# Kernel tuning notes

Measured on AMD Instinct MI355X. Metric: run time of the kernel, lower is better.

## Reference

```python
import jax, jax.numpy as jnp
import numpy as np

N = 50000      # nodes
E = 800000     # edges (before self-loops)
IN = 64        # in_dim
C = 64         # hidden_dim (per-head out channels)
H = 4          # heads
NEG_SLOPE = 0.2


def setup_inputs() -> dict:
    key = jax.random.key(0)
    ks = jax.random.split(key, 9)
    x = jax.random.normal(ks[0], (N, IN), jnp.float32)
    edge_index = jax.random.randint(ks[1], (2, E), 0, N)
    edge_attr = jax.random.uniform(ks[2], (E, 1), jnp.float32)
    s_in = 1.0 / np.sqrt(IN)
    s_c = 1.0 / np.sqrt(C)
    W = jax.random.normal(ks[3], (IN, H * C), jnp.float32) * s_in
    att_src = jax.random.normal(ks[4], (H, C), jnp.float32) * s_c
    att_dst = jax.random.normal(ks[5], (H, C), jnp.float32) * s_c
    lin_edge_w = jax.random.normal(ks[6], (1, H * C), jnp.float32)
    att_edge = jax.random.normal(ks[7], (H, C), jnp.float32) * s_c
    bias = jnp.zeros((C,), jnp.float32)
    return dict(x=x, edge_index=edge_index, edge_attr=edge_attr, W=W,
                att_src=att_src, att_dst=att_dst, lin_edge_w=lin_edge_w,
                att_edge=att_edge, bias=bias)


def reference(x, edge_index, edge_attr, W, att_src, att_dst, lin_edge_w, att_edge, bias):
    n = x.shape[0]
    # add self-loops (PyG default add_self_loops=True, fill_value='mean')
    loop = jnp.arange(n)
    src = jnp.concatenate([edge_index[0], loop])          # [E+N]
    dst = jnp.concatenate([edge_index[1], loop])          # [E+N]
    ea = jnp.concatenate([edge_attr,
                          jnp.full((n, 1), edge_attr.mean(), edge_attr.dtype)], axis=0)
    # node transform: [N, H, C]
    h = (x @ W).reshape(n, H, C)
    a_src = jnp.einsum('nhc,hc->nh', h, att_src)          # [N, H]
    a_dst = jnp.einsum('nhc,hc->nh', h, att_dst)          # [N, H]
    eh = (ea @ lin_edge_w).reshape(-1, H, C)              # [E+N, H, C]
    a_edge = jnp.einsum('ehc,hc->eh', eh, att_edge)       # [E+N, H]
    # per-edge attention logit
    alpha = a_src[src] + a_dst[dst] + a_edge              # [E+N, H]
    alpha = jax.nn.leaky_relu(alpha, NEG_SLOPE)
    # segment softmax over edges grouped by destination node
    amax = jax.ops.segment_max(alpha, dst, num_segments=n)
    alpha = jnp.exp(alpha - amax[dst])
    asum = jax.ops.segment_sum(alpha, dst, num_segments=n)
    alpha = alpha / (asum[dst] + 1e-16)                   # [E+N, H]
    # weighted message + scatter-add aggregation
    msg = h[src] * alpha[..., None]                       # [E+N, H, C]
    out = jax.ops.segment_sum(msg, dst, num_segments=n)   # [N, H, C]
    out = out.mean(axis=1) + bias                         # concat=False -> head mean
    # ReLU + residual
    return jax.nn.relu(out) + x
```

## Files before the change

kernel.cpp:

```cpp
#include <hip/hip_runtime.h>
#include <hip/hip_fp16.h>
#include <math.h>

#define H 4
#define C 64
#define HC 256
#define NEG 0.2f
#define ROWU 64
#define MAXREC 63
#define XPAD 72
#define HPAD 264
#define BKT 128
#define BSH 7
#define TILE 2048
#define SEG 32
#define SEGSH 5
#define G1 768

typedef __attribute__((ext_vector_type(8))) _Float16 half8;
typedef __attribute__((ext_vector_type(4))) float f32x4;
typedef float f32x2 __attribute__((vector_size(8)));

__global__ __launch_bounds__(256) void scatter_kernel(
    const int* __restrict__ ei, const float* __restrict__ edge_attr,
    uint2* __restrict__ arena, unsigned* __restrict__ counts,
    float* __restrict__ mean_acc, int Nn, int Ee, int ntile) {
    __shared__ float red[256];
    __shared__ unsigned cntA[512];
    int t = threadIdx.x;
    int nbkt = (Nn + BKT - 1) >> BSH;
    int tile = (int)blockIdx.x;
    for (int bb = t; bb < nbkt; bb += 256) cntA[bb] = 0;
    __syncthreads();
    int e0 = tile * TILE;
    size_t tbase = (size_t)tile * nbkt;
    float s = 0.f;
#pragma unroll 4
    for (int k = 0; k < TILE / 256; ++k) {
        int i = e0 + k * 256 + t;
        if (i < Ee) {
            int src = ei[i];
            int dst = ei[Ee + i];
            float ea = edge_attr[i];
            s += ea;
            unsigned q = (unsigned)(ea * 65535.f + 0.5f);
            int b = dst >> BSH;
            unsigned r = atomicAdd(&cntA[b], 1u);
            if (r < SEG)
                arena[(tbase + b) * SEG + r] =
                    make_uint2((q << 16) | (unsigned)src,
                               (unsigned)(dst & (BKT - 1)));
        }
    }
    __syncthreads();
    for (int bb = t; bb < nbkt; bb += 256) {
        unsigned c = cntA[bb];
        counts[tbase + bb] = c < (unsigned)SEG ? c : (unsigned)SEG;
    }
    red[t] = s;
    __syncthreads();
    for (int o = 128; o; o >>= 1) {
        if (t < o) red[t] += red[t + o];
        __syncthreads();
    }
    if (t == 0) atomicAdd(mean_acc, red[0]);
}

__global__ __launch_bounds__(256) void fused_kernel(
    const float* __restrict__ x, const float* __restrict__ W,
    const float* __restrict__ att_src, const float* __restrict__ att_dst,
    unsigned char* __restrict__ h, float* __restrict__ a_src, float* __restrict__ a_dst,
    const uint2* __restrict__ arena, const unsigned* __restrict__ counts,
    unsigned* __restrict__ edges, int Nn, int ntile, int nbkt) {
    __shared__ __align__(16) char smem[BKT * ROWU * 4 + BKT * 4 + 1024];
    int t = threadIdx.x;
    if ((int)blockIdx.x < G1) {
        _Float16* xs = (_Float16*)smem;
        _Float16* hs = (_Float16*)(smem + 16 * XPAD * 2);
        int w = t >> 6, lane = t & 63, quad = lane >> 4, c16 = lane & 15;
        half8 bf[4][2];
#pragma unroll
        for (int nt = 0; nt < 4; ++nt)
#pragma unroll
            for (int kh = 0; kh < 2; ++kh)
#pragma unroll
                for (int j = 0; j < 8; ++j)
                    bf[nt][kh][j] = (_Float16)W[(kh * 32 + quad * 8 + j) * HC +
                                                w * 64 + nt * 16 + c16];
        float ats[4], atd[4];
#pragma unroll
        for (int nt = 0; nt < 4; ++nt) {
            ats[nt] = att_src[w * 64 + nt * 16 + c16];
            atd[nt] = att_dst[w * 64 + nt * 16 + c16];
        }

        int nTiles = (Nn + 15) >> 4;
        for (int mt = blockIdx.x; mt < nTiles; mt += G1) {
            __syncthreads();
            {
                int row = t >> 4, col4 = (t & 15) * 4;
                int node = mt * 16 + row;
                float4 v = make_float4(0.f, 0.f, 0.f, 0.f);
                if (node < Nn) v = *(const float4*)(x + (size_t)node * 64 + col4);
                _Float16* dst = xs + row * XPAD + col4;
                dst[0] = (_Float16)v.x; dst[1] = (_Float16)v.y;
                dst[2] = (_Float16)v.z; dst[3] = (_Float16)v.w;
            }
            __syncthreads();
            half8 a0 = *(const half8*)(xs + c16 * XPAD + quad * 8);
            half8 a1 = *(const half8*)(xs + c16 * XPAD + 32 + quad * 8);
            f32x4 d[4];
#pragma unroll
            for (int nt = 0; nt < 4; ++nt) {
                f32x4 acc = {0.f, 0.f, 0.f, 0.f};
                acc = __builtin_amdgcn_mfma_f32_16x16x32_f16(a0, bf[nt][0], acc, 0, 0, 0);
                acc = __builtin_amdgcn_mfma_f32_16x16x32_f16(a1, bf[nt][1], acc, 0, 0, 0);
                d[nt] = acc;
            }
#pragma unroll
            for (int reg = 0; reg < 4; ++reg) {
                float ps = 0.f, pd = 0.f;
#pragma unroll
                for (int nt = 0; nt < 4; ++nt) {
                    ps += d[nt][reg] * ats[nt];
                    pd += d[nt][reg] * atd[nt];
                }
                ps += __shfl_xor(ps, 1); pd += __shfl_xor(pd, 1);
                ps += __shfl_xor(ps, 2); pd += __shfl_xor(pd, 2);
                ps += __shfl_xor(ps, 4); pd += __shfl_xor(pd, 4);
                ps += __shfl_xor(ps, 8); pd += __shfl_xor(pd, 8);
                if (c16 == 0) {
                    int node = mt * 16 + quad * 4 + reg;
                    if (node < Nn) {
                        a_src[node * 4 + w] = ps;
                        a_dst[node * 4 + w] = pd;
                    }
                }
            }
#pragma unroll
            for (int nt = 0; nt < 4; ++nt)
#pragma unroll
                for (int reg = 0; reg < 4; ++reg)
                    hs[(quad * 4 + reg) * HPAD + w * 64 + nt * 16 + c16] =
                        (_Float16)d[nt][reg];
            __syncthreads();
            {
                int row = t >> 4, chunk = t & 15;
                int node = mt * 16 + row;
                if (node < Nn) {
                    const uint4* sp = (const uint4*)(hs + row * HPAD + chunk * 16);
                    uint4 sA = sp[0], sB = sp[1];
                    unsigned ua[8] = {sA.x, sA.y, sA.z, sA.w, sB.x, sB.y, sB.z, sB.w};
                    unsigned ow[4];
#pragma unroll
                    for (int q = 0; q < 4; ++q) {
                        float2 p0 = __half22float2(*reinterpret_cast<const __half2*>(&ua[q * 2]));
                        float2 p1 = __half22float2(*reinterpret_cast<const __half2*>(&ua[q * 2 + 1]));
                        int v = __builtin_amdgcn_cvt_pk_fp8_f32(p0.x, p0.y, 0, false);
                        v = __builtin_amdgcn_cvt_pk_fp8_f32(p1.x, p1.y, v, true);
                        ow[q] = (unsigned)v;
                    }
                    *(uint4*)(h + (size_t)node * HC + chunk * 16) =
                        make_uint4(ow[0], ow[1], ow[2], ow[3]);
                }
            }
        }
    } else {
        unsigned* rows = (unsigned*)smem;
        unsigned* cnt = (unsigned*)(smem + BKT * ROWU * 4);
        unsigned short* segc = (unsigned short*)(smem + BKT * ROWU * 4 + BKT * 4);
        int b = (int)blockIdx.x - G1;
        if (t < BKT) cnt[t] = 0;
        for (int j = t; j < ntile; j += 256)
            segc[j] = (unsigned short)counts[(size_t)j * nbkt + b];
        __syncthreads();
        int total = ntile * SEG;
        for (int j = t; j < total; j += 256) {
            int seg = j >> SEGSH, slot = j & (SEG - 1);
            if (slot < (int)segc[seg]) {
                uint2 e = arena[((size_t)seg * nbkt + b) * SEG + slot];
                unsigned r = atomicAdd(&cnt[e.y], 1u);
                if (r < MAXREC) rows[e.y * ROWU + 1 + r] = e.x;
            }
        }
        __syncthreads();
        if (t < BKT) rows[t * ROWU] = cnt[t] < (unsigned)MAXREC ? cnt[t] : (unsigned)MAXREC;
        __syncthreads();
        size_t obase = (size_t)b * (BKT * ROWU);
        for (int i = t; i < BKT * (ROWU / 4); i += 256)
            *(uint4*)(edges + obase + i * 4) = *(const uint4*)(rows + i * 4);
    }
}

__global__ __launch_bounds__(256) void aggregate_kernel(
    const unsigned* __restrict__ edges,
    const float* __restrict__ a_src, const float* __restrict__ a_dst,
    const float* __restrict__ lin_edge_w, const float* __restrict__ att_edge,
    const float* __restrict__ mean_acc, const unsigned char* __restrict__ h,
    const float* __restrict__ bias, const float* __restrict__ x,
    float* __restrict__ out, int Nn, float invE) {
    int lane = threadIdx.x & 63;
    int n = blockIdx.x * 4 + (threadIdx.x >> 6);
    if (n >= Nn) return;
    int head = lane >> 4;
    int sub = lane & 15;

    size_t rowbase = (size_t)n * ROWU;
    unsigned deg = edges[rowbase];
    unsigned rec = edges[rowbase + 1 + lane];
    const unsigned* h8 = (const unsigned*)h;
    unsigned sv = h8[(size_t)n * 64 + lane];
    float mean = mean_acc[0] * invE;
    float ad = a_dst[n * 4 + head];
    float asn = a_src[n * 4 + head];

    float kp = 0.f;
#pragma unroll
    for (int j = 0; j < 4; ++j) {
        int c = sub * 4 + j;
        kp += lin_edge_w[head * C + c] * att_edge[head * C + c];
    }
    kp += __shfl_xor(kp, 1);
    kp += __shfl_xor(kp, 2);
    kp += __shfl_xor(kp, 4);
    kp += __shfl_xor(kp, 8);
    float K = kp;
    const float DEQ = 1.0f / 65535.f;

    if (deg > MAXREC) deg = MAXREC;

    float wk0, wk1, wk2, wk3;
    {
        float wtmp[4];
#pragma unroll
        for (int k = 0; k < 4; ++k) {
            int e = sub + 16 * k;
            unsigned re = (unsigned)__shfl((int)rec, e);
            int se = (e < (int)deg) ? (int)(re & 0xFFFF) : 0;
            float lg = a_src[se * 4 + head] + ad + (float)(re >> 16) * DEQ * K;
            lg = lg > 0.f ? lg : NEG * lg;
            wtmp[k] = (e < (int)deg) ? __expf(lg) : 0.f;
        }
        wk0 = wtmp[0]; wk1 = wtmp[1]; wk2 = wtmp[2]; wk3 = wtmp[3];
    }
    float sw = (wk0 + wk1) + (wk2 + wk3);
    sw += __shfl_xor(sw, 1);
    sw += __shfl_xor(sw, 2);
    sw += __shfl_xor(sw, 4);
    sw += __shfl_xor(sw, 8);

    float ls = asn + ad + mean * K;
    ls = ls > 0.f ? ls : NEG * ls;
    float wsl = __expf(ls);
    f32x2 s01 = __builtin_amdgcn_cvt_pk_f32_fp8((int)sv, false);
    f32x2 s23 = __builtin_amdgcn_cvt_pk_f32_fp8((int)sv, true);
    float4 acc = make_float4(wsl * s01[0], wsl * s01[1], wsl * s23[0], wsl * s23[1]);
    float swgt = sw + wsl;
    int hb = lane & 48;

    for (int g = 0; g < (int)deg; g += 8) {
        int cnt = (int)deg - g;
        if (cnt > 8) cnt = 8;
        unsigned hv0 = 0, hv1 = 0, hv2 = 0, hv3 = 0, hv4 = 0, hv5 = 0, hv6 = 0, hv7 = 0;
#define GATH(u, dst)                                                          \
        if (u < cnt) {                                                        \
            unsigned r = (unsigned)__builtin_amdgcn_readlane((int)rec, g + u);\
            dst = h8[(size_t)(r & 0xFFFF) * 64 + lane];                       \
        }
        GATH(0, hv0) GATH(1, hv1) GATH(2, hv2) GATH(3, hv3)
        GATH(4, hv4) GATH(5, hv5) GATH(6, hv6) GATH(7, hv7)
#undef GATH
#define CONS(u, src)                                                          \
        if (u < cnt) {                                                        \
            int e = g + u;                                                    \
            int k = e >> 4;                                                   \
            float wsrc = (k == 0) ? wk0 : (k == 1) ? wk1 : (k == 2) ? wk2 : wk3; \
            float wg = __shfl(wsrc, hb | (e & 15));                           \
            f32x2 f01 = __builtin_amdgcn_cvt_pk_f32_fp8((int)src, false);     \
            f32x2 f23 = __builtin_amdgcn_cvt_pk_f32_fp8((int)src, true);      \
            acc.x += wg * f01[0]; acc.y += wg * f01[1];                       \
            acc.z += wg * f23[0]; acc.w += wg * f23[1];                       \
        }
        CONS(0, hv0) CONS(1, hv1) CONS(2, hv2) CONS(3, hv3)
        CONS(4, hv4) CONS(5, hv5) CONS(6, hv6) CONS(7, hv7)
#undef CONS
    }

    float inv = 1.f / (swgt + 1e-16f);
    acc.x *= inv; acc.y *= inv; acc.z *= inv; acc.w *= inv;

    acc.x += __shfl_xor(acc.x, 16);
    acc.y += __shfl_xor(acc.y, 16);
    acc.z += __shfl_xor(acc.z, 16);
    acc.w += __shfl_xor(acc.w, 16);
    acc.x += __shfl_xor(acc.x, 32);
    acc.y += __shfl_xor(acc.y, 32);
    acc.z += __shfl_xor(acc.z, 32);
    acc.w += __shfl_xor(acc.w, 32);
    if (lane < 16) {
        float4 b = ((const float4*)bias)[lane];
        float4 xv = ((const float4*)x)[(size_t)n * 16 + lane];
        float4 o;
        o.x = fmaxf(acc.x * 0.25f + b.x, 0.f) + xv.x;
        o.y = fmaxf(acc.y * 0.25f + b.y, 0.f) + xv.y;
        o.z = fmaxf(acc.z * 0.25f + b.z, 0.f) + xv.z;
        o.w = fmaxf(acc.w * 0.25f + b.w, 0.f) + xv.w;
        ((float4*)out)[(size_t)n * 16 + lane] = o;
    }
}

extern "C" void kernel_launch(void* const* d_in, const int* in_sizes, int n_in,
                              void* d_out, int out_size, void* d_ws, size_t ws_size,
                              hipStream_t stream) {
    const float* x = (const float*)d_in[0];
    const int* ei = (const int*)d_in[1];
    const float* edge_attr = (const float*)d_in[2];
    const float* W = (const float*)d_in[3];
    const float* att_src = (const float*)d_in[4];
    const float* att_dst = (const float*)d_in[5];
    const float* lin_edge_w = (const float*)d_in[6];
    const float* att_edge = (const float*)d_in[7];
    const float* bias = (const float*)d_in[8];
    float* out = (float*)d_out;
    int Nn = in_sizes[0] / 64;
    int Ee = in_sizes[1] / 2;
    int NB = (Nn + BKT - 1) >> BSH;
    int ntile = (Ee + TILE - 1) / TILE;

    char* p = (char*)d_ws;
    size_t off = 0;
    auto alloc = [&](size_t bytes) -> char* {
        char* r = p + off;
        off += (bytes + 255) & ~(size_t)255;
        return r;
    };
    float* mean_acc = (float*)alloc(256);
    size_t zero_bytes = off;
    unsigned* counts = (unsigned*)alloc((size_t)ntile * NB * 4);
    uint2* arena = (uint2*)alloc((size_t)ntile * NB * SEG * 8);
    unsigned* edges = (unsigned*)alloc((size_t)NB * BKT * ROWU * 4);
    unsigned char* h = (unsigned char*)alloc((size_t)Nn * HC);
    float* a_src = (float*)alloc((size_t)Nn * H * 4);
    float* a_dst = (float*)alloc((size_t)Nn * H * 4);
    (void)ws_size;

    hipMemsetAsync(d_ws, 0, zero_bytes, stream);
    scatter_kernel<<<ntile, 256, 0, stream>>>(ei, edge_attr, arena, counts,
                                              mean_acc, Nn, Ee, ntile);
    fused_kernel<<<G1 + NB, 256, 0, stream>>>(x, W, att_src, att_dst,
                                              h, a_src, a_dst, arena, counts,
                                              edges, Nn, ntile, NB);
    aggregate_kernel<<<(Nn + 3) / 4, 256, 0, stream>>>(edges, a_src, a_dst,
                                                       lin_edge_w, att_edge, mean_acc,
                                                       h, bias, x, out, Nn,
                                                       1.0f / (float)Ee);
}
```

Baseline: 167.7 us.

## Co-schedule node GEMM with edge scatter and drop LDS staging in GEMM

```diff
diff --git a/kernel.cpp b/kernel.cpp
--- a/kernel.cpp
+++ b/kernel.cpp
@@ -8,75 +8,26 @@
 #define NEG 0.2f
 #define ROWU 64
 #define MAXREC 63
-#define XPAD 72
-#define HPAD 264
 #define BKT 128
 #define BSH 7
 #define TILE 2048
 #define SEG 32
 #define SEGSH 5
-#define G1 768
+#define G1GEMM 1024
 
 typedef __attribute__((ext_vector_type(8))) _Float16 half8;
 typedef __attribute__((ext_vector_type(4))) float f32x4;
 typedef float f32x2 __attribute__((vector_size(8)));
 
-__global__ __launch_bounds__(256) void scatter_kernel(
+__global__ __launch_bounds__(256) void front_kernel(
+    const float* __restrict__ x, const float* __restrict__ W,
+    const float* __restrict__ att_src, const float* __restrict__ att_dst,
     const int* __restrict__ ei, const float* __restrict__ edge_attr,
+    unsigned char* __restrict__ h, float* __restrict__ a_src, float* __restrict__ a_dst,
     uint2* __restrict__ arena, unsigned* __restrict__ counts,
     float* __restrict__ mean_acc, int Nn, int Ee, int ntile) {
-    __shared__ float red[256];
-    __shared__ unsigned cntA[512];
     int t = threadIdx.x;
-    int nbkt = (Nn + BKT - 1) >> BSH;
-    int tile = (int)blockIdx.x;
-    for (int bb = t; bb < nbkt; bb += 256) cntA[bb] = 0;
-    __syncthreads();
-    int e0 = tile * TILE;
-    size_t tbase = (size_t)tile * nbkt;
-    float s = 0.f;
-#pragma unroll 4
-    for (int k = 0; k < TILE / 256; ++k) {
-        int i = e0 + k * 256 + t;
-        if (i < Ee) {
-            int src = ei[i];
-            int dst = ei[Ee + i];
-            float ea = edge_attr[i];
-            s += ea;
-            unsigned q = (unsigned)(ea * 65535.f + 0.5f);
-            int b = dst >> BSH;
-            unsigned r = atomicAdd(&cntA[b], 1u);
-            if (r < SEG)
-                arena[(tbase + b) * SEG + r] =
-                    make_uint2((q << 16) | (unsigned)src,
-                               (unsigned)(dst & (BKT - 1)));
-        }
-    }
-    __syncthreads();
-    for (int bb = t; bb < nbkt; bb += 256) {
-        unsigned c = cntA[bb];
-        counts[tbase + bb] = c < (unsigned)SEG ? c : (unsigned)SEG;
-    }
-    red[t] = s;
-    __syncthreads();
-    for (int o = 128; o; o >>= 1) {
-        if (t < o) red[t] += red[t + o];
-        __syncthreads();
-    }
-    if (t == 0) atomicAdd(mean_acc, red[0]);
-}
-
-__global__ __launch_bounds__(256) void fused_kernel(
-    const float* __restrict__ x, const float* __restrict__ W,
-    const float* __restrict__ att_src, const float* __restrict__ att_dst,
-    unsigned char* __restrict__ h, float* __restrict__ a_src, float* __restrict__ a_dst,
-    const uint2* __restrict__ arena, const unsigned* __restrict__ counts,
-    unsigned* __restrict__ edges, int Nn, int ntile, int nbkt) {
-    __shared__ __align__(16) char smem[BKT * ROWU * 4 + BKT * 4 + 1024];
-    int t = threadIdx.x;
-    if ((int)blockIdx.x < G1) {
-        _Float16* xs = (_Float16*)smem;
-        _Float16* hs = (_Float16*)(smem + 16 * XPAD * 2);
+    if ((int)blockIdx.x < G1GEMM) {
         int w = t >> 6, lane = t & 63, quad = lane >> 4, c16 = lane & 15;
         half8 bf[4][2];
 #pragma unroll
@@ -93,22 +44,29 @@
             ats[nt] = att_src[w * 64 + nt * 16 + c16];
             atd[nt] = att_dst[w * 64 + nt * 16 + c16];
         }
-
-        int nTiles = (Nn + 15) >> 4;
-        for (int mt = blockIdx.x; mt < nTiles; mt += G1) {
-            __syncthreads();
-            {
-                int row = t >> 4, col4 = (t & 15) * 4;
-                int node = mt * 16 + row;
-                float4 v = make_float4(0.f, 0.f, 0.f, 0.f);
-                if (node < Nn) v = *(const float4*)(x + (size_t)node * 64 + col4);
-                _Float16* dst = xs + row * XPAD + col4;
-                dst[0] = (_Float16)v.x; dst[1] = (_Float16)v.y;
-                dst[2] = (_Float16)v.z; dst[3] = (_Float16)v.w;
+        unsigned* h32 = (unsigned*)h;
+
+        int nT = (Nn + 15) >> 4;
+        for (int mt = blockIdx.x; mt < nT; mt += G1GEMM) {
+            int anode = mt * 16 + c16;
+            half8 a0, a1;
+#pragma unroll
+            for (int j = 0; j < 8; ++j) { a0[j] = (_Float16)0.f; a1[j] = (_Float16)0.f; }
+            if (anode < Nn) {
+                const float* xr = x + (size_t)anode * 64 + quad * 8;
+                float4 p0 = *(const float4*)xr;
+                float4 p1 = *(const float4*)(xr + 4);
+                float4 q0 = *(const float4*)(xr + 32);
+                float4 q1 = *(const float4*)(xr + 36);
+                a0[0] = (_Float16)p0.x; a0[1] = (_Float16)p0.y;
+                a0[2] = (_Float16)p0.z; a0[3] = (_Float16)p0.w;
+                a0[4] = (_Float16)p1.x; a0[5] = (_Float16)p1.y;
+                a0[6] = (_Float16)p1.z; a0[7] = (_Float16)p1.w;
+                a1[0] = (_Float16)q0.x; a1[1] = (_Float16)q0.y;
+                a1[2] = (_Float16)q0.z; a1[3] = (_Float16)q0.w;
+                a1[4] = (_Float16)q1.x; a1[5] = (_Float16)q1.y;
+                a1[6] = (_Float16)q1.z; a1[7] = (_Float16)q1.w;
             }
-            __syncthreads();
-            half8 a0 = *(const half8*)(xs + c16 * XPAD + quad * 8);
-            half8 a1 = *(const half8*)(xs + c16 * XPAD + 32 + quad * 8);
             f32x4 d[4];
 #pragma unroll
             for (int nt = 0; nt < 4; ++nt) {
@@ -119,6 +77,7 @@
             }
 #pragma unroll
             for (int reg = 0; reg < 4; ++reg) {
+                int node = mt * 16 + quad * 4 + reg;
                 float ps = 0.f, pd = 0.f;
 #pragma unroll
                 for (int nt = 0; nt < 4; ++nt) {
@@ -129,67 +88,85 @@
                 ps += __shfl_xor(ps, 2); pd += __shfl_xor(pd, 2);
                 ps += __shfl_xor(ps, 4); pd += __shfl_xor(pd, 4);
                 ps += __shfl_xor(ps, 8); pd += __shfl_xor(pd, 8);
-                if (c16 == 0) {
-                    int node = mt * 16 + quad * 4 + reg;
-                    if (node < Nn) {
+                if (node < Nn) {
+                    if (c16 == 0) {
                         a_src[node * 4 + w] = ps;
                         a_dst[node * 4 + w] = pd;
                     }
+                    int v = __builtin_amdgcn_cvt_pk_fp8_f32(d[0][reg], d[1][reg], 0, false);
+                    v = __builtin_amdgcn_cvt_pk_fp8_f32(d[2][reg], d[3][reg], v, true);
+                    h32[(size_t)node * 64 + w * 16 + c16] = (unsigned)v;
                 }
             }
-#pragma unroll
-            for (int nt = 0; nt < 4; ++nt)
-#pragma unroll
-                for (int reg = 0; reg < 4; ++reg)
-                    hs[(quad * 4 + reg) * HPAD + w * 64 + nt * 16 + c16] =
-                        (_Float16)d[nt][reg];
+        }
+    } else {
+        __shared__ float red[256];
+        __shared__ unsigned cntA[512];
+        int nbkt = (Nn + BKT - 1) >> BSH;
+        int tile = (int)blockIdx.x - G1GEMM;
+        for (int bb = t; bb < nbkt; bb += 256) cntA[bb] = 0;
+        __syncthreads();
+        int e0 = tile * TILE;
+        size_t tbase = (size_t)tile * nbkt;
+        float s = 0.f;
+#pragma unroll 4
+        for (int k = 0; k < TILE / 256; ++k) {
+            int i = e0 + k * 256 + t;
+            if (i < Ee) {
+                int src = ei[i];
+                int dst = ei[Ee + i];
+                float ea = edge_attr[i];
+                s += ea;
+                unsigned q = (unsigned)(ea * 65535.f + 0.5f);
+                int b = dst >> BSH;
+                unsigned r = atomicAdd(&cntA[b], 1u);
+                if (r < SEG)
+                    arena[(tbase + b) * SEG + r] =
+                        make_uint2((q << 16) | (unsigned)src,
+                                   (unsigned)(dst & (BKT - 1)));
+            }
+        }
+        __syncthreads();
+        for (int bb = t; bb < nbkt; bb += 256) {
+            unsigned c = cntA[bb];
+            counts[tbase + bb] = c < (unsigned)SEG ? c : (unsigned)SEG;
+        }
+        red[t] = s;
+        __syncthreads();
+        for (int o = 128; o; o >>= 1) {
+            if (t < o) red[t] += red[t + o];
             __syncthreads();
-            {
-                int row = t >> 4, chunk = t & 15;
-                int node = mt * 16 + row;
-                if (node < Nn) {
-                    const uint4* sp = (const uint4*)(hs + row * HPAD + chunk * 16);
-                    uint4 sA = sp[0], sB = sp[1];
-                    unsigned ua[8] = {sA.x, sA.y, sA.z, sA.w, sB.x, sB.y, sB.z, sB.w};
-                    unsigned ow[4];
-#pragma unroll
-                    for (int q = 0; q < 4; ++q) {
-                        float2 p0 = __half22float2(*reinterpret_cast<const __half2*>(&ua[q * 2]));
-                        float2 p1 = __half22float2(*reinterpret_cast<const __half2*>(&ua[q * 2 + 1]));
-                        int v = __builtin_amdgcn_cvt_pk_fp8_f32(p0.x, p0.y, 0, false);
-                        v = __builtin_amdgcn_cvt_pk_fp8_f32(p1.x, p1.y, v, true);
-                        ow[q] = (unsigned)v;
-                    }
-                    *(uint4*)(h + (size_t)node * HC + chunk * 16) =
-                        make_uint4(ow[0], ow[1], ow[2], ow[3]);
-                }
-            }
-        }
-    } else {
-        unsigned* rows = (unsigned*)smem;
-        unsigned* cnt = (unsigned*)(smem + BKT * ROWU * 4);
-        unsigned short* segc = (unsigned short*)(smem + BKT * ROWU * 4 + BKT * 4);
-        int b = (int)blockIdx.x - G1;
-        if (t < BKT) cnt[t] = 0;
-        for (int j = t; j < ntile; j += 256)
-            segc[j] = (unsigned short)counts[(size_t)j * nbkt + b];
-        __syncthreads();
-        int total = ntile * SEG;
-        for (int j = t; j < total; j += 256) {
-            int seg = j >> SEGSH, slot = j & (SEG - 1);
-            if (slot < (int)segc[seg]) {
-                uint2 e = arena[((size_t)seg * nbkt + b) * SEG + slot];
-                unsigned r = atomicAdd(&cnt[e.y], 1u);
-                if (r < MAXREC) rows[e.y * ROWU + 1 + r] = e.x;
-            }
-        }
-        __syncthreads();
-        if (t < BKT) rows[t * ROWU] = cnt[t] < (unsigned)MAXREC ? cnt[t] : (unsigned)MAXREC;
-        __syncthreads();
-        size_t obase = (size_t)b * (BKT * ROWU);
-        for (int i = t; i < BKT * (ROWU / 4); i += 256)
-            *(uint4*)(edges + obase + i * 4) = *(const uint4*)(rows + i * 4);
-    }
+        }
+        if (t == 0) atomicAdd(mean_acc, red[0]);
+    }
+}
+
+__global__ __launch_bounds__(256) void bucket_kernel(
+    const uint2* __restrict__ arena, const unsigned* __restrict__ counts,
+    unsigned* __restrict__ edges, int ntile, int nbkt) {
+    __shared__ unsigned rows[BKT * ROWU];
+    __shared__ unsigned cnt[BKT];
+    __shared__ unsigned short segc[512];
+    int b = blockIdx.x, t = threadIdx.x;
+    if (t < BKT) cnt[t] = 0;
+    for (int j = t; j < ntile; j += 256)
+        segc[j] = (unsigned short)counts[(size_t)j * nbkt + b];
+    __syncthreads();
+    int total = ntile * SEG;
+    for (int j = t; j < total; j += 256) {
+        int seg = j >> SEGSH, slot = j & (SEG - 1);
+        if (slot < (int)segc[seg]) {
+            uint2 e = arena[((size_t)seg * nbkt + b) * SEG + slot];
+            unsigned r = atomicAdd(&cnt[e.y], 1u);
+            if (r < MAXREC) rows[e.y * ROWU + 1 + r] = e.x;
+        }
+    }
+    __syncthreads();
+    if (t < BKT) rows[t * ROWU] = cnt[t] < (unsigned)MAXREC ? cnt[t] : (unsigned)MAXREC;
+    __syncthreads();
+    size_t obase = (size_t)b * (BKT * ROWU);
+    for (int i = t; i < BKT * (ROWU / 4); i += 256)
+        *(uint4*)(edges + obase + i * 4) = *(const uint4*)(rows + i * 4);
 }
 
 __global__ __launch_bounds__(256) void aggregate_kernel(
@@ -298,14 +275,16 @@
     acc.z += __shfl_xor(acc.z, 32);
     acc.w += __shfl_xor(acc.w, 32);
     if (lane < 16) {
-        float4 b = ((const float4*)bias)[lane];
-        float4 xv = ((const float4*)x)[(size_t)n * 16 + lane];
-        float4 o;
-        o.x = fmaxf(acc.x * 0.25f + b.x, 0.f) + xv.x;
-        o.y = fmaxf(acc.y * 0.25f + b.y, 0.f) + xv.y;
-        o.z = fmaxf(acc.z * 0.25f + b.z, 0.f) + xv.z;
-        o.w = fmaxf(acc.w * 0.25f + b.w, 0.f) + xv.w;
-        ((float4*)out)[(size_t)n * 16 + lane] = o;
+        float av0 = acc.x, av1 = acc.y, av2 = acc.z, av3 = acc.w;
+        float b0 = bias[lane], b1 = bias[16 + lane];
+        float b2 = bias[32 + lane], b3 = bias[48 + lane];
+        const float* xr = x + (size_t)n * 64 + lane;
+        float x0 = xr[0], x1 = xr[16], x2 = xr[32], x3 = xr[48];
+        float* orow = out + (size_t)n * 64 + lane;
+        orow[0]  = fmaxf(av0 * 0.25f + b0, 0.f) + x0;
+        orow[16] = fmaxf(av1 * 0.25f + b1, 0.f) + x1;
+        orow[32] = fmaxf(av2 * 0.25f + b2, 0.f) + x2;
+        orow[48] = fmaxf(av3 * 0.25f + b3, 0.f) + x3;
     }
 }
 
@@ -345,11 +324,11 @@
     (void)ws_size;
 
     hipMemsetAsync(d_ws, 0, zero_bytes, stream);
-    scatter_kernel<<<ntile, 256, 0, stream>>>(ei, edge_attr, arena, counts,
-                                              mean_acc, Nn, Ee, ntile);
-    fused_kernel<<<G1 + NB, 256, 0, stream>>>(x, W, att_src, att_dst,
-                                              h, a_src, a_dst, arena, counts,
-                                              edges, Nn, ntile, NB);
+    front_kernel<<<G1GEMM + ntile, 256, 0, stream>>>(x, W, att_src, att_dst,
+                                                     ei, edge_attr, h, a_src, a_dst,
+                                                     arena, counts, mean_acc,
+                                                     Nn, Ee, ntile);
+    bucket_kernel<<<NB, 256, 0, stream>>>(arena, counts, edges, ntile, NB);
     aggregate_kernel<<<(Nn + 3) / 4, 256, 0, stream>>>(edges, a_src, a_dst,
                                                        lin_edge_w, att_edge, mean_acc,
                                                        h, bias, x, out, Nn,
```

After: 166.1 us. Within noise of the previous version (-1.0%).
